# Performance work log

Hardware: AMD Instinct MI355X
Metric: run time of the kernel (lower is better)

The kernel has to match this reference:

```python
import jax, jax.numpy as jnp
import numpy as np

WEIGHT = 0.1
TEMPERATURE = 0.07
EPS_NORM = 1e-12   # F.normalize eps
EPS_DEN = 1e-6     # denominator eps in pos_mask.sum()


def setup_inputs() -> dict:
    key = jax.random.key(0)
    k1, k2 = jax.random.split(key)
    features = jax.random.normal(k1, (4, 1000, 2048), dtype=jnp.float32)
    target = jax.random.randint(k2, (4, 1000), 0, 16, dtype=jnp.int64)
    return {"features": features, "target": target}


def _per_sample_loss(f, t):
    # f: [N, C], t: [N]
    N = f.shape[0]
    # F.normalize(dim=1)
    norm = jnp.maximum(jnp.linalg.norm(f, axis=1, keepdims=True), EPS_NORM)
    f = f / norm
    # [N, N] cosine similarities scaled by temperature
    sim = jnp.matmul(f, f.T) / TEMPERATURE
    eye = jnp.eye(N, dtype=f.dtype)
    pos = (t[:, None] == t[None, :]).astype(f.dtype) * (1.0 - eye)
    neg = 1.0 - pos - eye
    pos_sim = sim * pos
    # -log(exp(pos_sim) / (exp(pos_sim) + sum_j exp(sim)*neg))  summed over ALL entries
    denom = jnp.exp(pos_sim) + jnp.sum(jnp.exp(sim) * neg, axis=1, keepdims=True)
    loss_mat = jnp.log(denom) - pos_sim
    pos_sum = pos.sum()
    return loss_mat.sum() / (pos_sum + EPS_DEN), pos_sum


def reference(features, target):
    # features: [B, N, C] (already 3-D: no subsampling / interpolation paths fire)
    losses, pos_sums = jax.vmap(_per_sample_loss)(features, target)
    valid = pos_sums > 0
    num_pairs = valid.sum().astype(features.dtype)
    total = jnp.where(valid, losses, 0.0).sum()
    return jnp.where(num_pairs > 0, WEIGHT * total / num_pairs,
                     jnp.asarray(WEIGHT * 0.1, dtype=features.dtype))
```

## Files before the change

kernel.cpp:

```cpp
#include <hip/hip_runtime.h>
#include <hip/hip_fp8.h>
#include <math.h>

#define BB 4
#define NN 1000
#define NP 1024
#define CC 2048
#define TINV (1.0f / 0.07f)
#define BK 64
#define FS 8.0f

#define FNORM_BYTES ((size_t)BB * NP * CC)
#define SIMB_BYTES  ((size_t)2 * BB * NP * NP)
#define RL_BYTES    ((size_t)BB * NP * 4)

typedef unsigned char u8;
typedef float  f32x4  __attribute__((ext_vector_type(4)));
typedef float  f32x16 __attribute__((ext_vector_type(16)));

__device__ __forceinline__ void load_lds16(const void* g, void* l) {
    __builtin_amdgcn_global_load_lds(
        (const __attribute__((address_space(1))) unsigned int*)g,
        (__attribute__((address_space(3))) unsigned int*)l, 16, 0, 0);
}

__device__ __forceinline__ float blk_sum(float v, volatile float* lds) {
    int lane = threadIdx.x & 63;
    int wid  = threadIdx.x >> 6;
#pragma unroll
    for (int off = 32; off; off >>= 1) v += __shfl_down(v, off);
    __syncthreads();
    if (lane == 0) lds[wid] = v;
    __syncthreads();
    return lds[0] + lds[1] + lds[2] + lds[3];
}

__device__ __forceinline__ float wave_sum(float v) {
#pragma unroll
    for (int off = 32; off; off >>= 1) v += __shfl_down(v, off);
    return __shfl(v, 0);
}

__device__ __forceinline__ float fp8_to_f32(u8 b) {
    __hip_fp8_e4m3 q; q.__x = b;
    return (float)q;
}

__global__ __launch_bounds__(256) void norm_fp8_kernel(const float* __restrict__ f,
                                                       u8* __restrict__ out) {
    __shared__ float lds[4];
    __shared__ float scale_s;
    const int blk = blockIdx.x;
    const int b = blk >> 10, r = blk & (NP - 1);
    u8* dst = out + ((size_t)b * NP + r) * CC;
    const int tid = threadIdx.x;

    if (r >= NN) {
        ((uint2*)dst)[tid] = make_uint2(0u, 0u);
        return;
    }
    const float* src = f + ((size_t)b * NN + r) * CC;

    float ss = 0.f;
#pragma unroll
    for (int h = 0; h < 2; ++h) {
        float4 v = ((const float4*)src)[tid + h * 256];
        ss += v.x * v.x + v.y * v.y + v.z * v.z + v.w * v.w;
    }
    float tot = blk_sum(ss, lds);
    if (tid == 0) scale_s = FS / fmaxf(sqrtf(tot), 1e-12f);
    __syncthreads();
    const float sc = scale_s;

    float4 v0 = ((const float4*)src)[tid * 2];
    float4 v1 = ((const float4*)src)[tid * 2 + 1];
    float x[8] = {v0.x, v0.y, v0.z, v0.w, v1.x, v1.y, v1.z, v1.w};
    union { u8 b[8]; uint2 u; } pk;
#pragma unroll
    for (int k = 0; k < 8; ++k) {
        __hip_fp8_e4m3 q(x[k] * sc);
        pk.b[k] = q.__x;
    }
    ((uint2*)dst)[tid] = pk.u;
}

__global__ __launch_bounds__(256) void simgemm_mfma(const u8* __restrict__ fn,
                                                    u8* __restrict__ simb) {
    __shared__ __align__(16) u8 As0[128 * BK], As1[128 * BK];
    __shared__ __align__(16) u8 Bs0[128 * BK], Bs1[128 * BK];

    const int bz = blockIdx.z;
    const int b  = bz >> 1;
    const int kbeg = (bz & 1) * (CC / 2);
    const int tI = blockIdx.y * 128;
    const int tJ = blockIdx.x * 128;
    const u8* base = fn + (size_t)b * NP * CC;
    u8* S = simb + (size_t)bz * NP * NP;

    const int tid  = threadIdx.x;
    const int wid  = tid >> 6;
    const int lane = tid & 63;
    const int wm   = wid >> 1;
    const int wn   = wid & 1;
    const int ln32 = lane & 31;
    const int kh   = lane >> 5;
    const int sw   = (ln32 >> 1) & 3;

    const int srow   = tid >> 2;
    const int schunk = (tid & 3) ^ ((srow >> 1) & 3);
    const u8* gA = base + (size_t)(tI + srow) * CC + kbeg + schunk * 16;
    const u8* gB = base + (size_t)(tJ + srow) * CC + kbeg + schunk * 16;
    const int wvoff = wid * 1024;

    f32x16 acc[2][2] = {};

#define STAGE(k0, A, B)                                            \
    {                                                              \
        load_lds16(gA + (k0),                   (A) + wvoff);      \
        load_lds16(gA + (k0) + (size_t)64 * CC, (A) + 4096 + wvoff); \
        load_lds16(gB + (k0),                   (B) + wvoff);      \
        load_lds16(gB + (k0) + (size_t)64 * CC, (B) + 4096 + wvoff); \
    }

#define COMPUTE(A, B)                                                         \
    {                                                                         \
        _Pragma("unroll")                                                     \
        for (int kc = 0; kc < 4; ++kc) {                                      \
            const int co = ((kc ^ sw) * 16) + kh * 8;                         \
            long a0 = *(const long*)&(A)[(wm * 64      + ln32) * BK + co];    \
            long a1 = *(const long*)&(A)[(wm * 64 + 32 + ln32) * BK + co];    \
            long b0 = *(const long*)&(B)[(wn * 64      + ln32) * BK + co];    \
            long b1 = *(const long*)&(B)[(wn * 64 + 32 + ln32) * BK + co];    \
            acc[0][0] = __builtin_amdgcn_mfma_f32_32x32x16_fp8_fp8(a0, b0, acc[0][0], 0, 0, 0); \
            acc[0][1] = __builtin_amdgcn_mfma_f32_32x32x16_fp8_fp8(a0, b1, acc[0][1], 0, 0, 0); \
            acc[1][0] = __builtin_amdgcn_mfma_f32_32x32x16_fp8_fp8(a1, b0, acc[1][0], 0, 0, 0); \
            acc[1][1] = __builtin_amdgcn_mfma_f32_32x32x16_fp8_fp8(a1, b1, acc[1][1], 0, 0, 0); \
        }                                                                     \
    }

    STAGE(0, As0, Bs0);
#pragma unroll 1
    for (int k0 = 0; k0 < CC / 2; k0 += 2 * BK) {
        __syncthreads();
        if (k0 + BK < CC / 2) STAGE(k0 + BK, As1, Bs1);
        COMPUTE(As0, Bs0);
        __syncthreads();
        if (k0 + 2 * BK < CC / 2) STAGE(k0 + 2 * BK, As0, Bs0);
        COMPUTE(As1, Bs1);
    }
#undef STAGE
#undef COMPUTE

    const float oscale = TINV / (FS * FS);
#pragma unroll
    for (int at = 0; at < 2; ++at) {
#pragma unroll
        for (int bt = 0; bt < 2; ++bt) {
            const int col = tJ + wn * 64 + bt * 32 + ln32;
#pragma unroll
            for (int r = 0; r < 16; ++r) {
                const int row = tI + wm * 64 + at * 32 + (r & 3) + 8 * (r >> 2) + 4 * kh;
                __hip_fp8_e4m3 q(acc[at][bt][r] * oscale);
                S[(size_t)row * NP + col] = q.__x;
            }
        }
    }
}

__global__ __launch_bounds__(256) void rowloss_kernel(const u8* __restrict__ simb,
                                                      const int* __restrict__ tgt,
                                                      float* __restrict__ rloss,
                                                      float* __restrict__ rpos) {
    __shared__ __align__(16) int ts[NN];
    __shared__ float rowv[4][NP];
    const int b = blockIdx.y;
    const int wid = threadIdx.x >> 6, lane = threadIdx.x & 63;
    const int* t = tgt + (size_t)b * NN;
    for (int j = threadIdx.x; j < NN; j += 256) ts[j] = t[j];
    __syncthreads();

    const int i = blockIdx.x * 4 + wid;
    const u8* r0 = simb + (size_t)(2 * b) * NP * NP + (size_t)i * NP;
    const u8* r1 = r0 + (size_t)NP * NP;
    const int ti = ts[i];

    float sneg = 0.f, pcnt = 0.f;
    for (int g = lane; g < NN / 8; g += 64) {
        union { uint2 u; u8 b[8]; } pa, pb;
        pa.u = ((const uint2*)r0)[g];
        pb.u = ((const uint2*)r1)[g];
        float v[8];
#pragma unroll
        for (int k = 0; k < 8; ++k) v[k] = fp8_to_f32(pa.b[k]) + fp8_to_f32(pb.b[k]);
        *(f32x4*)&rowv[wid][g * 8]     = *(f32x4*)&v[0];
        *(f32x4*)&rowv[wid][g * 8 + 4] = *(f32x4*)&v[4];
        const int jb = g * 8;
#pragma unroll
        for (int k = 0; k < 8; ++k) {
            const int j = jb + k;
            if (j != i) {
                if (ts[j] == ti) pcnt += 1.f;
                else             sneg += __expf(v[k]);
            }
        }
    }
    const float Sv = wave_sum(sneg);
    const float p  = wave_sum(pcnt);

    float term = 0.f;
    for (int g = lane; g < NN / 8; g += 64) {
        const int jb = g * 8;
        float v[8];
        *(f32x4*)&v[0] = *(const f32x4*)&rowv[wid][jb];
        *(f32x4*)&v[4] = *(const f32x4*)&rowv[wid][jb + 4];
#pragma unroll
        for (int k = 0; k < 8; ++k) {
            const int j = jb + k;
            if (j != i && ts[j] == ti)
                term += __logf(__expf(v[k]) + Sv) - v[k];
        }
    }
    const float tt = wave_sum(term);
    if (lane == 0) {
        rloss[b * NP + i] = tt + ((float)NN - p) * __logf(1.f + Sv);
        rpos [b * NP + i] = p;
    }
}

__global__ __launch_bounds__(256) void final_kernel(const float* __restrict__ rloss,
                                                    const float* __restrict__ rpos,
                                                    float* __restrict__ out) {
    __shared__ float lds[4];
    float total = 0.f, np = 0.f;
    for (int b = 0; b < BB; ++b) {
        float l = 0.f, p = 0.f;
        for (int i = threadIdx.x; i < NN; i += 256) {
            l += rloss[b * NP + i];
            p += rpos [b * NP + i];
        }
        float ls = blk_sum(l, lds);
        float ps = blk_sum(p, lds);
        if (ps > 0.f) { total += ls / (ps + 1e-6f); np += 1.f; }
    }
    if (threadIdx.x == 0)
        out[0] = (np > 0.f) ? 0.1f * total / np : 0.1f * 0.1f;
}

extern "C" void kernel_launch(void* const* d_in, const int* in_sizes, int n_in,
                              void* d_out, int out_size, void* d_ws, size_t ws_size,
                              hipStream_t stream) {
    const float* feat = (const float*)d_in[0];
    const int*   tgt  = (const int*)d_in[1];
    char* ws = (char*)d_ws;
    u8*    fnorm = (u8*)ws;                       ws += FNORM_BYTES;
    u8*    simb  = (u8*)ws;                       ws += SIMB_BYTES;
    float* rloss = (float*)ws;                    ws += RL_BYTES;
    float* rpos  = (float*)ws;

    norm_fp8_kernel<<<dim3(BB * NP), 256, 0, stream>>>(feat, fnorm);
    simgemm_mfma<<<dim3(NP / 128, NP / 128, 2 * BB), 256, 0, stream>>>(fnorm, simb);
    rowloss_kernel<<<dim3(NN / 4, BB), 256, 0, stream>>>(simb, tgt, rloss, rpos);
    final_kernel<<<1, 256, 0, stream>>>(rloss, rpos, (float*)d_out);
}
```

Before: 113.4 us.

## Fuse row-loss reductions into the similarity GEMM epilogue and drop split-K

The GEMM epilogue now computes the exp of negative similarities and adds them per row with atomics. Positive-pair similarities go into a fixed 128-slot per-row buffer, so the FP8 similarity matrix is no longer written to memory and read back. Split-K over two halves is removed; each block computes the full K with 512 threads and eight 64x32 warp tiles. This removes the intermediate matrix traffic and the re-decode pass. The costs are fewer blocks, float atomics in the epilogue, and a cap on positives per row that assumes labels are spread out enough.

```diff
diff --git a/kernel.cpp b/kernel.cpp
--- a/kernel.cpp
+++ b/kernel.cpp
@@ -9,9 +9,12 @@
 #define TINV (1.0f / 0.07f)
 #define BK 64
 #define FS 8.0f
+#define PSLOTS 128
 
 #define FNORM_BYTES ((size_t)BB * NP * CC)
-#define SIMB_BYTES  ((size_t)2 * BB * NP * NP)
+#define SROW_BYTES  ((size_t)BB * NP * 4)
+#define PCNT_BYTES  ((size_t)BB * NP * 4)
+#define POSS_BYTES  ((size_t)BB * NP * PSLOTS * 4)
 #define RL_BYTES    ((size_t)BB * NP * 4)
 
 typedef unsigned char u8;
@@ -41,17 +44,15 @@
     return __shfl(v, 0);
 }
 
-__device__ __forceinline__ float fp8_to_f32(u8 b) {
-    __hip_fp8_e4m3 q; q.__x = b;
-    return (float)q;
-}
-
 __global__ __launch_bounds__(256) void norm_fp8_kernel(const float* __restrict__ f,
-                                                       u8* __restrict__ out) {
+                                                       u8* __restrict__ out,
+                                                       float* __restrict__ Srow,
+                                                       int* __restrict__ pcnt) {
     __shared__ float lds[4];
     __shared__ float scale_s;
     const int blk = blockIdx.x;
     const int b = blk >> 10, r = blk & (NP - 1);
+    if (threadIdx.x == 0) { Srow[blk] = 0.f; pcnt[blk] = 0; }
     u8* dst = out + ((size_t)b * NP + r) * CC;
     const int tid = threadIdx.x;
 
@@ -84,42 +85,44 @@
     ((uint2*)dst)[tid] = pk.u;
 }
 
-__global__ __launch_bounds__(256) void simgemm_mfma(const u8* __restrict__ fn,
-                                                    u8* __restrict__ simb) {
+__global__ __launch_bounds__(512) void simgemm_fused(const u8* __restrict__ fn,
+                                                     const int* __restrict__ tgt,
+                                                     float* __restrict__ Srow,
+                                                     int* __restrict__ pcnt,
+                                                     float* __restrict__ pos_s) {
     __shared__ __align__(16) u8 As0[128 * BK], As1[128 * BK];
     __shared__ __align__(16) u8 Bs0[128 * BK], Bs1[128 * BK];
-
-    const int bz = blockIdx.z;
-    const int b  = bz >> 1;
-    const int kbeg = (bz & 1) * (CC / 2);
+    __shared__ __align__(16) int ts[NN];
+
+    const int b  = blockIdx.z;
     const int tI = blockIdx.y * 128;
     const int tJ = blockIdx.x * 128;
     const u8* base = fn + (size_t)b * NP * CC;
-    u8* S = simb + (size_t)bz * NP * NP;
 
     const int tid  = threadIdx.x;
     const int wid  = tid >> 6;
     const int lane = tid & 63;
-    const int wm   = wid >> 1;
-    const int wn   = wid & 1;
+    const int wm   = wid >> 2;
+    const int wn   = wid & 3;
     const int ln32 = lane & 31;
     const int kh   = lane >> 5;
     const int sw   = (ln32 >> 1) & 3;
 
     const int srow   = tid >> 2;
     const int schunk = (tid & 3) ^ ((srow >> 1) & 3);
-    const u8* gA = base + (size_t)(tI + srow) * CC + kbeg + schunk * 16;
-    const u8* gB = base + (size_t)(tJ + srow) * CC + kbeg + schunk * 16;
+    const u8* gA = base + (size_t)(tI + srow) * CC + schunk * 16;
+    const u8* gB = base + (size_t)(tJ + srow) * CC + schunk * 16;
     const int wvoff = wid * 1024;
 
-    f32x16 acc[2][2] = {};
-
-#define STAGE(k0, A, B)                                            \
-    {                                                              \
-        load_lds16(gA + (k0),                   (A) + wvoff);      \
-        load_lds16(gA + (k0) + (size_t)64 * CC, (A) + 4096 + wvoff); \
-        load_lds16(gB + (k0),                   (B) + wvoff);      \
-        load_lds16(gB + (k0) + (size_t)64 * CC, (B) + 4096 + wvoff); \
+    const int* t = tgt + (size_t)b * NN;
+    for (int j = tid; j < NN; j += 512) ts[j] = t[j];
+
+    f32x16 acc[2] = {};
+
+#define STAGE(k0, A, B)                                 \
+    {                                                   \
+        load_lds16(gA + (k0), (A) + wvoff);             \
+        load_lds16(gB + (k0), (B) + wvoff);             \
     }
 
 #define COMPUTE(A, B)                                                         \
@@ -129,101 +132,76 @@
             const int co = ((kc ^ sw) * 16) + kh * 8;                         \
             long a0 = *(const long*)&(A)[(wm * 64      + ln32) * BK + co];    \
             long a1 = *(const long*)&(A)[(wm * 64 + 32 + ln32) * BK + co];    \
-            long b0 = *(const long*)&(B)[(wn * 64      + ln32) * BK + co];    \
-            long b1 = *(const long*)&(B)[(wn * 64 + 32 + ln32) * BK + co];    \
-            acc[0][0] = __builtin_amdgcn_mfma_f32_32x32x16_fp8_fp8(a0, b0, acc[0][0], 0, 0, 0); \
-            acc[0][1] = __builtin_amdgcn_mfma_f32_32x32x16_fp8_fp8(a0, b1, acc[0][1], 0, 0, 0); \
-            acc[1][0] = __builtin_amdgcn_mfma_f32_32x32x16_fp8_fp8(a1, b0, acc[1][0], 0, 0, 0); \
-            acc[1][1] = __builtin_amdgcn_mfma_f32_32x32x16_fp8_fp8(a1, b1, acc[1][1], 0, 0, 0); \
+            long b0 = *(const long*)&(B)[(wn * 32      + ln32) * BK + co];    \
+            acc[0] = __builtin_amdgcn_mfma_f32_32x32x16_fp8_fp8(a0, b0, acc[0], 0, 0, 0); \
+            acc[1] = __builtin_amdgcn_mfma_f32_32x32x16_fp8_fp8(a1, b0, acc[1], 0, 0, 0); \
         }                                                                     \
     }
 
     STAGE(0, As0, Bs0);
 #pragma unroll 1
-    for (int k0 = 0; k0 < CC / 2; k0 += 2 * BK) {
+    for (int k0 = 0; k0 < CC; k0 += 2 * BK) {
         __syncthreads();
-        if (k0 + BK < CC / 2) STAGE(k0 + BK, As1, Bs1);
+        if (k0 + BK < CC) STAGE(k0 + BK, As1, Bs1);
         COMPUTE(As0, Bs0);
         __syncthreads();
-        if (k0 + 2 * BK < CC / 2) STAGE(k0 + 2 * BK, As0, Bs0);
+        if (k0 + 2 * BK < CC) STAGE(k0 + 2 * BK, As0, Bs0);
         COMPUTE(As1, Bs1);
     }
 #undef STAGE
 #undef COMPUTE
 
     const float oscale = TINV / (FS * FS);
+    const int col_g = tJ + wn * 32 + ln32;
+    const int tc = (col_g < NN) ? ts[col_g] : -1;
+    float* Srow_b = Srow + (size_t)b * NP;
+    int*   pcnt_b = pcnt + (size_t)b * NP;
+
 #pragma unroll
     for (int at = 0; at < 2; ++at) {
 #pragma unroll
-        for (int bt = 0; bt < 2; ++bt) {
-            const int col = tJ + wn * 64 + bt * 32 + ln32;
-#pragma unroll
-            for (int r = 0; r < 16; ++r) {
-                const int row = tI + wm * 64 + at * 32 + (r & 3) + 8 * (r >> 2) + 4 * kh;
-                __hip_fp8_e4m3 q(acc[at][bt][r] * oscale);
-                S[(size_t)row * NP + col] = q.__x;
+        for (int r = 0; r < 16; ++r) {
+            const int row_g = tI + wm * 64 + at * 32 + (r & 3) + 8 * (r >> 2) + 4 * kh;
+            const float s = acc[at][r] * oscale;
+            const bool rowok = (row_g < NN);
+            const int  tr = rowok ? ts[row_g] : -2;
+            const bool valid = rowok && (col_g < NN) && (row_g != col_g);
+            const bool ispos = valid && (tr == tc);
+            float v = (valid && !ispos) ? __expf(s) : 0.f;
+#pragma unroll
+            for (int off = 16; off; off >>= 1) v += __shfl_xor(v, off, 32);
+            if (ln32 == 0 && v != 0.f) atomicAdd(&Srow_b[row_g], v);
+            if (ispos) {
+                const int slot = atomicAdd(&pcnt_b[row_g], 1);
+                if (slot < PSLOTS)
+                    pos_s[((size_t)b * NP + row_g) * PSLOTS + slot] = s;
             }
         }
     }
 }
 
-__global__ __launch_bounds__(256) void rowloss_kernel(const u8* __restrict__ simb,
-                                                      const int* __restrict__ tgt,
+__global__ __launch_bounds__(256) void posloss_kernel(const float* __restrict__ Srow,
+                                                      const int* __restrict__ pcnt,
+                                                      const float* __restrict__ pos_s,
                                                       float* __restrict__ rloss,
                                                       float* __restrict__ rpos) {
-    __shared__ __align__(16) int ts[NN];
-    __shared__ float rowv[4][NP];
     const int b = blockIdx.y;
     const int wid = threadIdx.x >> 6, lane = threadIdx.x & 63;
-    const int* t = tgt + (size_t)b * NN;
-    for (int j = threadIdx.x; j < NN; j += 256) ts[j] = t[j];
-    __syncthreads();
-
     const int i = blockIdx.x * 4 + wid;
-    const u8* r0 = simb + (size_t)(2 * b) * NP * NP + (size_t)i * NP;
-    const u8* r1 = r0 + (size_t)NP * NP;
-    const int ti = ts[i];
-
-    float sneg = 0.f, pcnt = 0.f;
-    for (int g = lane; g < NN / 8; g += 64) {
-        union { uint2 u; u8 b[8]; } pa, pb;
-        pa.u = ((const uint2*)r0)[g];
-        pb.u = ((const uint2*)r1)[g];
-        float v[8];
-#pragma unroll
-        for (int k = 0; k < 8; ++k) v[k] = fp8_to_f32(pa.b[k]) + fp8_to_f32(pb.b[k]);
-        *(f32x4*)&rowv[wid][g * 8]     = *(f32x4*)&v[0];
-        *(f32x4*)&rowv[wid][g * 8 + 4] = *(f32x4*)&v[4];
-        const int jb = g * 8;
-#pragma unroll
-        for (int k = 0; k < 8; ++k) {
-            const int j = jb + k;
-            if (j != i) {
-                if (ts[j] == ti) pcnt += 1.f;
-                else             sneg += __expf(v[k]);
-            }
-        }
-    }
-    const float Sv = wave_sum(sneg);
-    const float p  = wave_sum(pcnt);
+    const int idx = b * NP + i;
+    const float S = Srow[idx];
+    const int   p = pcnt[idx];
+    const float* ps = pos_s + (size_t)idx * PSLOTS;
 
     float term = 0.f;
-    for (int g = lane; g < NN / 8; g += 64) {
-        const int jb = g * 8;
-        float v[8];
-        *(f32x4*)&v[0] = *(const f32x4*)&rowv[wid][jb];
-        *(f32x4*)&v[4] = *(const f32x4*)&rowv[wid][jb + 4];
-#pragma unroll
-        for (int k = 0; k < 8; ++k) {
-            const int j = jb + k;
-            if (j != i && ts[j] == ti)
-                term += __logf(__expf(v[k]) + Sv) - v[k];
-        }
+    for (int k = lane; k < p; k += 64) {
+        const float s = ps[k];
+        term += __logf(__expf(s) + S) - s;
     }
     const float tt = wave_sum(term);
     if (lane == 0) {
-        rloss[b * NP + i] = tt + ((float)NN - p) * __logf(1.f + Sv);
-        rpos [b * NP + i] = p;
+        rloss[idx] = tt + ((float)NN - (float)p) * __logf(1.f + S);
+        rpos [idx] = (float)p;
     }
 }
 
@@ -253,12 +231,14 @@
     const int*   tgt  = (const int*)d_in[1];
     char* ws = (char*)d_ws;
     u8*    fnorm = (u8*)ws;                       ws += FNORM_BYTES;
-    u8*    simb  = (u8*)ws;                       ws += SIMB_BYTES;
+    float* Srow  = (float*)ws;                    ws += SROW_BYTES;
+    int*   pcnt  = (int*)ws;                      ws += PCNT_BYTES;
+    float* pos_s = (float*)ws;                    ws += POSS_BYTES;
     float* rloss = (float*)ws;                    ws += RL_BYTES;
     float* rpos  = (float*)ws;
 
-    norm_fp8_kernel<<<dim3(BB * NP), 256, 0, stream>>>(feat, fnorm);
-    simgemm_mfma<<<dim3(NP / 128, NP / 128, 2 * BB), 256, 0, stream>>>(fnorm, simb);
-    rowloss_kernel<<<dim3(NN / 4, BB), 256, 0, stream>>>(simb, tgt, rloss, rpos);
+    norm_fp8_kernel<<<dim3(BB * NP), 256, 0, stream>>>(feat, fnorm, Srow, pcnt);
+    simgemm_fused<<<dim3(NP / 128, NP / 128, BB), 512, 0, stream>>>(fnorm, tgt, Srow, pcnt, pos_s);
+    posloss_kernel<<<dim3(NN / 4, BB), 256, 0, stream>>>(Srow, pcnt, pos_s, rloss, rpos);
     final_kernel<<<1, 256, 0, stream>>>(rloss, rpos, (float*)d_out);
 }
```

Result: slower. 136.8 us (+20.7%).
